# Kernel optimization log

Measured on AMD Instinct MI355X. Metric: run time of the kernel, lower is better.

The kernel has to match this reference:

```python
import jax, jax.numpy as jnp
import numpy as np

E = 8      # num_experts
D = 1024   # input_size
H = 1024   # head_size
K = 2      # top-k


def setup_inputs() -> dict:
    key = jax.random.key(0)
    k1, k2, k3, k4, k5, k6 = jax.random.split(key, 6)
    x = jax.random.normal(k1, (4, 1024, D), dtype=jnp.float32)
    # ParallelExperts init: uniform(-1/fan_in, 1/fan_in)
    w1 = jax.random.uniform(k2, (E, D, H), jnp.float32, -1.0 / D, 1.0 / D)
    b1 = jax.random.uniform(k3, (E, H), jnp.float32, -1.0 / np.sqrt(D), 1.0 / np.sqrt(D))
    w2 = jax.random.uniform(k4, (E, H, D), jnp.float32, -1.0 / H, 1.0 / H)
    b2 = jax.random.uniform(k5, (E, D), jnp.float32, -1.0 / np.sqrt(H), 1.0 / np.sqrt(H))
    # gate Linear(input_size, num_experts, bias=False); scaled so softmax isn't saturated
    wg = jax.random.normal(k6, (D, E), dtype=jnp.float32) * 0.02
    return {"x": x, "w1": w1, "b1": b1, "w2": w2, "b2": b2, "wg": wg}


def reference(x, w1, b1, w2, b2, wg):
    bsz, length, d = x.shape
    xf = x.reshape(-1, d)                                  # [T, D]
    # --- top_k_gating (noisy_gating=False, no skip_mask) ---
    logits = xf @ wg                                       # [T, E]
    probs = jax.nn.softmax(logits, axis=-1)
    top_v, top_i = jax.lax.top_k(probs, K)                 # [T, K]
    top_v = top_v / (jnp.sum(top_v, axis=-1, keepdims=True) + 1e-6)
    # dense combine weights: gate[t, e] = renormalized prob if e in top-k else 0
    gates = jnp.sum(jax.nn.one_hot(top_i, E, dtype=xf.dtype) * top_v[..., None], axis=1)  # [T, E]
    # --- map: per-expert first GEMM + bias (dense formulation == grouped GEMM, no drops) ---
    h = jnp.einsum('td,edh->teh', xf, w1) + b1[None]       # [T, E, H]
    # --- activation between map and reduce (nn.GELU, exact erf form) ---
    a = jax.nn.gelu(h, approximate=False)
    # --- reduce: per-expert second GEMM + bias, scaled by gate, scatter-add back ---
    o = jnp.einsum('teh,ehd->ted', a, w2) + b2[None]       # [T, E, D]
    y = jnp.einsum('te,ted->td', gates, o)                 # [T, D]
    return y.reshape(bsz, length, d)
```

## Files before the change

### kernel.cpp

```cpp
#include <hip/hip_runtime.h>
#include <hip/hip_bf16.h>
#include <math.h>

#define TT 4096
#define EE 8
#define DD 1024
#define HH 1024
#define CAP 4096

typedef __attribute__((ext_vector_type(8))) short bf16x8;
typedef __attribute__((ext_vector_type(4))) float f32x4;

#define GLL16(gp, lp)                                                                   \
    __builtin_amdgcn_global_load_lds((__attribute__((address_space(1))) void*)(gp),     \
                                     (__attribute__((address_space(3))) void*)(lp),     \
                                     16, 0, 0)

static const size_t OFF_XB     = 0;
static const size_t OFF_W1T    = 8u * 1024 * 1024;
static const size_t OFF_W2T    = 24u * 1024 * 1024;
static const size_t OFF_ABUF   = 40u * 1024 * 1024;
static const size_t OFF_OBUF   = 56u * 1024 * 1024;
static const size_t OFF_ROWMAP = 88u * 1024 * 1024;
static const size_t OFF_GATES  = OFF_ROWMAP + 8 * CAP * 4;
static const size_t OFF_COUNTS = OFF_GATES + 8192 * 4;
static const size_t OFF_PICKS  = OFF_COUNTS + 256;

#define NGATE 1024

__global__ __launch_bounds__(256) void prep_kernel(
    const float* __restrict__ x, const float* __restrict__ wg,
    const float* __restrict__ w1, const float* __restrict__ w2,
    __hip_bfloat16* __restrict__ xb,
    __hip_bfloat16* __restrict__ w1t, __hip_bfloat16* __restrict__ w2t,
    int* __restrict__ picks, float* __restrict__ gates)
{
    __shared__ float tl[64][65];
    const int bid = blockIdx.x;
    const int tid = threadIdx.x;

    if (bid >= NGATE) {
        const int bt = bid - NGATE;
        const int mat = bt >> 8;
        const int tt = bt & 255;
        const int R = (tt >> 4) * 64;
        const int C = (tt & 15) * 64;
        const float* src = (mat < EE ? w1 : w2) + (size_t)(mat & 7) * DD * HH;
        __hip_bfloat16* dst = (mat < EE ? w1t : w2t) + (size_t)(mat & 7) * DD * HH;

        const int lrow = tid >> 4;
        const int c4 = tid & 15;
#pragma unroll
        for (int i = 0; i < 4; ++i) {
            const int r = lrow + i * 16;
            float4 v = *(const float4*)(src + (size_t)(R + r) * 1024 + C + c4 * 4);
            tl[r][c4 * 4 + 0] = v.x;
            tl[r][c4 * 4 + 1] = v.y;
            tl[r][c4 * 4 + 2] = v.z;
            tl[r][c4 * 4 + 3] = v.w;
        }
        __syncthreads();
        const int seg = tid & 7;
        const int orow0 = tid >> 3;
#pragma unroll
        for (int p = 0; p < 2; ++p) {
            const int orow = orow0 + p * 32;
            unsigned short u[8];
#pragma unroll
            for (int j = 0; j < 8; ++j) {
                __hip_bfloat16 h = __float2bfloat16(tl[seg * 8 + j][orow]);
                u[j] = *(unsigned short*)&h;
            }
            *(ushort4*)(dst + (size_t)(C + orow) * 1024 + R + seg * 8)     = (ushort4){u[0], u[1], u[2], u[3]};
            *(ushort4*)(dst + (size_t)(C + orow) * 1024 + R + seg * 8 + 4) = (ushort4){u[4], u[5], u[6], u[7]};
        }
        return;
    }

    const int lane = tid & 63;
    const int wave = tid >> 6;
    const int t = bid * 4 + wave;
    {
        const float4* xr = (const float4*)(x + (size_t)t * DD);
        ushort4* xbr = (ushort4*)(xb + (size_t)t * DD);

        float acc[EE];
#pragma unroll
        for (int e = 0; e < EE; ++e) acc[e] = 0.f;

#pragma unroll
        for (int c = 0; c < 4; ++c) {
            const int v4 = lane + 64 * c;
            float4 xv = xr[v4];
            __hip_bfloat16 h0 = __float2bfloat16(xv.x);
            __hip_bfloat16 h1 = __float2bfloat16(xv.y);
            __hip_bfloat16 h2 = __float2bfloat16(xv.z);
            __hip_bfloat16 h3 = __float2bfloat16(xv.w);
            ushort4 s;
            s.x = *(unsigned short*)&h0; s.y = *(unsigned short*)&h1;
            s.z = *(unsigned short*)&h2; s.w = *(unsigned short*)&h3;
            xbr[v4] = s;
            const float4* wrow = (const float4*)(wg + (size_t)(4 * v4) * EE);
            const float xs[4] = {xv.x, xv.y, xv.z, xv.w};
#pragma unroll
            for (int q = 0; q < 4; ++q) {
                float4 w0 = wrow[q * 2];
                float4 w1v = wrow[q * 2 + 1];
                acc[0] = fmaf(xs[q], w0.x, acc[0]);
                acc[1] = fmaf(xs[q], w0.y, acc[1]);
                acc[2] = fmaf(xs[q], w0.z, acc[2]);
                acc[3] = fmaf(xs[q], w0.w, acc[3]);
                acc[4] = fmaf(xs[q], w1v.x, acc[4]);
                acc[5] = fmaf(xs[q], w1v.y, acc[5]);
                acc[6] = fmaf(xs[q], w1v.z, acc[6]);
                acc[7] = fmaf(xs[q], w1v.w, acc[7]);
            }
        }
#pragma unroll
        for (int off = 32; off > 0; off >>= 1) {
#pragma unroll
            for (int e = 0; e < EE; ++e) acc[e] += __shfl_xor(acc[e], off, 64);
        }
        if (lane == 0) {
            float mx = acc[0];
#pragma unroll
            for (int e = 1; e < EE; ++e) mx = fmaxf(mx, acc[e]);
            float p[EE];
            float s = 0.f;
#pragma unroll
            for (int e = 0; e < EE; ++e) { p[e] = expf(acc[e] - mx); s += p[e]; }
            int i0 = 0;
#pragma unroll
            for (int e = 1; e < EE; ++e) if (acc[e] > acc[i0]) i0 = e;
            int i1 = (i0 == 0) ? 1 : 0;
#pragma unroll
            for (int e = 0; e < EE; ++e) {
                if (e != i0 && acc[e] > acc[i1]) i1 = e;
            }
            float v0 = p[i0] / s, v1 = p[i1] / s;
            float den = v0 + v1 + 1e-6f;
            gates[t * 2 + 0] = v0 / den;
            gates[t * 2 + 1] = v1 / den;
            picks[t] = i0 | (i1 << 4);
        }
    }
}

__global__ __launch_bounds__(256) void bucket_build(
    const int* __restrict__ picks, int* __restrict__ rowmap, int* __restrict__ counts)
{
    const int e = blockIdx.x;
    const int tid = threadIdx.x;
    const int lane = tid & 63;
    const int wave = tid >> 6;
    __shared__ int wsum[4];

    int runtot = 0;
    for (int tb = 0; tb < TT; tb += 256) {
        const int t = tb + tid;
        const int p = picks[t];
        const int m0 = ((p & 15) == e) ? 1 : 0;
        const int m1 = (((p >> 4) & 15) == e) ? 1 : 0;
        const int c = m0 + m1;
        int incl = c;
#pragma unroll
        for (int off = 1; off < 64; off <<= 1) {
            int v = __shfl_up(incl, off, 64);
            if (lane >= off) incl += v;
        }
        if (lane == 63) wsum[wave] = incl;
        __syncthreads();
        int wbase = 0;
#pragma unroll
        for (int w = 0; w < 4; ++w) wbase += (w < wave) ? wsum[w] : 0;
        int slot = runtot + wbase + incl - c;
        if (m0) { rowmap[e * CAP + slot] = t * 2; slot += 1; }
        if (m1) { rowmap[e * CAP + slot] = t * 2 + 1; }
        runtot += wsum[0] + wsum[1] + wsum[2] + wsum[3];
        __syncthreads();
    }
    if (tid == 0) counts[e] = runtot;
}

template <int LAYER>
__global__ __launch_bounds__(512) void moe_gemm(
    const __hip_bfloat16* __restrict__ Abase,
    const __hip_bfloat16* __restrict__ Bbase,
    const float* __restrict__ bias,
    const int* __restrict__ rowmap,
    const int* __restrict__ counts,
    const float* __restrict__ gates,
    void* __restrict__ OutP)
{
    const int bid = blockIdx.x;
    const int e = bid & 7;
    const int n0 = ((bid >> 3) & 7) * 128;
    const int m0 = (bid >> 6) * 128;
    const int cnt = counts[e];
    if (m0 >= cnt) return;
    const int tid = threadIdx.x;
    const int lane = tid & 63;
    const int wave = tid >> 6;
    const int wm = (wave >> 2) * 64;
    const int wn = (wave & 3) * 32;
    const int lrow = lane & 15;
    const int quad = lane >> 4;

    __shared__ __hip_bfloat16 As[2][128 * 32];
    __shared__ __hip_bfloat16 Bs[2][128 * 32];

    const int ar = m0 + (tid >> 2);
    const int ea = rowmap[e * CAP + (ar < cnt ? ar : 0)];
    const size_t srcA = (size_t)(LAYER == 1 ? (ea >> 1) : ea);
    const __hip_bfloat16* gA = Abase + srcA * DD + (tid & 3) * 8;
    const __hip_bfloat16* Bexp = Bbase + (size_t)e * DD * HH;
    const __hip_bfloat16* gB = Bexp + (size_t)(n0 + (tid >> 2)) * DD + (tid & 3) * 8;

    f32x4 acc[4][2];
#pragma unroll
    for (int i = 0; i < 4; ++i)
#pragma unroll
        for (int j = 0; j < 2; ++j) acc[i][j] = (f32x4){0.f, 0.f, 0.f, 0.f};

    for (int kt = 0; kt < DD / 64; ++kt) {
#pragma unroll
        for (int s = 0; s < 2; ++s) {
            const int ko = kt * 64 + s * 32;
            GLL16(gA + ko, (char*)&As[s][0] + wave * 1024);
            GLL16(gB + ko, (char*)&Bs[s][0] + wave * 1024);
        }
        __syncthreads();

#pragma unroll
        for (int s = 0; s < 2; ++s) {
            const bf16x8* Av = (const bf16x8*)&As[s][0];
            const bf16x8* Bv = (const bf16x8*)&Bs[s][0];
            bf16x8 af[4], bfr[2];
#pragma unroll
            for (int i = 0; i < 4; ++i)
                af[i] = Av[(wm + i * 16 + lrow) * 4 + quad];
#pragma unroll
            for (int i = 0; i < 2; ++i)
                bfr[i] = Bv[(wn + i * 16 + lrow) * 4 + quad];
#pragma unroll
            for (int mi = 0; mi < 4; ++mi)
#pragma unroll
                for (int ni = 0; ni < 2; ++ni)
                    acc[mi][ni] = __builtin_amdgcn_mfma_f32_16x16x32_bf16(
                        af[mi], bfr[ni], acc[mi][ni], 0, 0, 0);
        }
        __syncthreads();
    }

    if (LAYER == 1) {
        __hip_bfloat16* abuf = (__hip_bfloat16*)OutP;
#pragma unroll
        for (int mi = 0; mi < 4; ++mi) {
#pragma unroll
            for (int r = 0; r < 4; ++r) {
                const int mrow = wm + mi * 16 + quad * 4 + r;
                const int gm = m0 + mrow;
                if (gm < cnt) {
                    const int ent = rowmap[e * CAP + gm];
                    __hip_bfloat16* orow = abuf + (size_t)ent * HH + n0 + wn + lrow;
#pragma unroll
                    for (int ni = 0; ni < 2; ++ni) {
                        float v = acc[mi][ni][r] + bias[e * HH + n0 + wn + ni * 16 + lrow];
                        v = 0.5f * v * (1.f + erff(v * 0.70710678118654752f));
                        orow[ni * 16] = __float2bfloat16(v);
                    }
                }
            }
        }
    } else {
        float* obuf = (float*)OutP;
#pragma unroll
        for (int mi = 0; mi < 4; ++mi) {
#pragma unroll
            for (int r = 0; r < 4; ++r) {
                const int mrow = wm + mi * 16 + quad * 4 + r;
                const int gm = m0 + mrow;
                if (gm < cnt) {
                    const int ent = rowmap[e * CAP + gm];
                    const float g = gates[ent];
                    float* orow = obuf + (size_t)ent * DD + n0 + wn + lrow;
#pragma unroll
                    for (int ni = 0; ni < 2; ++ni) {
                        float v = acc[mi][ni][r] + bias[e * DD + n0 + wn + ni * 16 + lrow];
                        orow[ni * 16] = v * g;
                    }
                }
            }
        }
    }
}

__global__ __launch_bounds__(256) void combine_kernel(
    const float* __restrict__ obuf, float* __restrict__ y)
{
    const size_t i = (size_t)blockIdx.x * 256 + threadIdx.x;
    const size_t t = i >> 8;
    const size_t c = i & 255;
    const float4* o0 = (const float4*)(obuf + t * 2 * DD);
    float4 a = o0[c];
    float4 b = o0[256 + c];
    float4 r;
    r.x = a.x + b.x; r.y = a.y + b.y; r.z = a.z + b.z; r.w = a.w + b.w;
    ((float4*)y)[i] = r;
}

extern "C" void kernel_launch(void* const* d_in, const int* in_sizes, int n_in,
                              void* d_out, int out_size, void* d_ws, size_t ws_size,
                              hipStream_t stream)
{
    const float* x  = (const float*)d_in[0];
    const float* w1 = (const float*)d_in[1];
    const float* b1 = (const float*)d_in[2];
    const float* w2 = (const float*)d_in[3];
    const float* b2 = (const float*)d_in[4];
    const float* wg = (const float*)d_in[5];
    float* y = (float*)d_out;

    char* ws = (char*)d_ws;
    __hip_bfloat16* xb   = (__hip_bfloat16*)(ws + OFF_XB);
    __hip_bfloat16* w1t  = (__hip_bfloat16*)(ws + OFF_W1T);
    __hip_bfloat16* w2t  = (__hip_bfloat16*)(ws + OFF_W2T);
    __hip_bfloat16* abuf = (__hip_bfloat16*)(ws + OFF_ABUF);
    float* obuf  = (float*)(ws + OFF_OBUF);
    int*   rowmap = (int*)(ws + OFF_ROWMAP);
    float* gates  = (float*)(ws + OFF_GATES);
    int*   counts = (int*)(ws + OFF_COUNTS);
    int*   picks  = (int*)(ws + OFF_PICKS);

    prep_kernel<<<NGATE + 4096, 256, 0, stream>>>(x, wg, w1, w2, xb, w1t, w2t, picks, gates);
    bucket_build<<<EE, 256, 0, stream>>>(picks, rowmap, counts);
    moe_gemm<1><<<(CAP / 128) * 8 * EE, 512, 0, stream>>>(
        xb, w1t, b1, rowmap, counts, gates, (void*)abuf);
    moe_gemm<2><<<(CAP / 128) * 8 * EE, 512, 0, stream>>>(
        abuf, w2t, b2, rowmap, counts, gates, (void*)obuf);
    combine_kernel<<<TT * DD / 4 / 256, 256, 0, stream>>>(obuf, y);
}
```

Baseline: 214.3 us.

## Double-buffer LDS tiles in expert GEMM and vectorize transpose stores

The expert GEMM now uses two LDS buffers. It issues the global-to-LDS loads for the next K tile right after the barrier, so they can overlap the MFMA work on the current tile, and it drops one barrier per iteration. The weight-transpose path also writes eight bf16 values with a single 16-byte store instead of two 8-byte stores. LDS use per block doubles, which may lower occupancy. The compiler may also insert conservative waits on the async LDS loads before the ds_reads, which would limit the overlap.

```diff
diff --git a/kernel.cpp b/kernel.cpp
--- a/kernel.cpp
+++ b/kernel.cpp
@@ -10,6 +10,7 @@
 
 typedef __attribute__((ext_vector_type(8))) short bf16x8;
 typedef __attribute__((ext_vector_type(4))) float f32x4;
+typedef __attribute__((ext_vector_type(8))) unsigned short ushort8;
 
 #define GLL16(gp, lp)                                                                   \
     __builtin_amdgcn_global_load_lds((__attribute__((address_space(1))) void*)(gp),     \
@@ -65,14 +66,13 @@
 #pragma unroll
         for (int p = 0; p < 2; ++p) {
             const int orow = orow0 + p * 32;
-            unsigned short u[8];
+            ushort8 u;
 #pragma unroll
             for (int j = 0; j < 8; ++j) {
                 __hip_bfloat16 h = __float2bfloat16(tl[seg * 8 + j][orow]);
                 u[j] = *(unsigned short*)&h;
             }
-            *(ushort4*)(dst + (size_t)(C + orow) * 1024 + R + seg * 8)     = (ushort4){u[0], u[1], u[2], u[3]};
-            *(ushort4*)(dst + (size_t)(C + orow) * 1024 + R + seg * 8 + 4) = (ushort4){u[4], u[5], u[6], u[7]};
+            *(ushort8*)(dst + (size_t)(C + orow) * 1024 + R + seg * 8) = u;
         }
         return;
     }
@@ -206,8 +206,8 @@
     const int lrow = lane & 15;
     const int quad = lane >> 4;
 
-    __shared__ __hip_bfloat16 As[2][128 * 32];
-    __shared__ __hip_bfloat16 Bs[2][128 * 32];
+    __shared__ __hip_bfloat16 As[2][2][128 * 32];
+    __shared__ __hip_bfloat16 Bs[2][2][128 * 32];
 
     const int ar = m0 + (tid >> 2);
     const int ea = rowmap[e * CAP + (ar < cnt ? ar : 0)];
@@ -222,19 +222,25 @@
 #pragma unroll
         for (int j = 0; j < 2; ++j) acc[i][j] = (f32x4){0.f, 0.f, 0.f, 0.f};
 
+#define STAGE(BUF, KT)                                                      \
+    {                                                                       \
+        _Pragma("unroll") for (int s = 0; s < 2; ++s) {                     \
+            const int ko = (KT) * 64 + s * 32;                              \
+            GLL16(gA + ko, (char*)&As[BUF][s][0] + wave * 1024);            \
+            GLL16(gB + ko, (char*)&Bs[BUF][s][0] + wave * 1024);            \
+        }                                                                   \
+    }
+
+    STAGE(0, 0);
     for (int kt = 0; kt < DD / 64; ++kt) {
+        const int cur = kt & 1;
+        __syncthreads();
+        if (kt < DD / 64 - 1) STAGE(cur ^ 1, kt + 1);
+
 #pragma unroll
         for (int s = 0; s < 2; ++s) {
-            const int ko = kt * 64 + s * 32;
-            GLL16(gA + ko, (char*)&As[s][0] + wave * 1024);
-            GLL16(gB + ko, (char*)&Bs[s][0] + wave * 1024);
-        }
-        __syncthreads();
-
-#pragma unroll
-        for (int s = 0; s < 2; ++s) {
-            const bf16x8* Av = (const bf16x8*)&As[s][0];
-            const bf16x8* Bv = (const bf16x8*)&Bs[s][0];
+            const bf16x8* Av = (const bf16x8*)&As[cur][s][0];
+            const bf16x8* Bv = (const bf16x8*)&Bs[cur][s][0];
             bf16x8 af[4], bfr[2];
 #pragma unroll
             for (int i = 0; i < 4; ++i)
@@ -249,8 +255,8 @@
                     acc[mi][ni] = __builtin_amdgcn_mfma_f32_16x16x32_bf16(
                         af[mi], bfr[ni], acc[mi][ni], 0, 0, 0);
         }
-        __syncthreads();
-    }
+    }
+#undef STAGE
 
     if (LAYER == 1) {
         __hip_bfloat16* abuf = (__hip_bfloat16*)OutP;
```

Measured after the change: 232.0 us. 1.08x slower.

## Overlap W2 transpose with layer-1 GEMM via extra blocks, widen stores

Applied to the files above, without the earlier changes.

The fp32-to-bf16 transpose of the second-layer weights moves out of the prep kernel. It now runs in extra blocks appended to the layer-1 MoE GEMM grid, so it can fill idle CUs, since many GEMM blocks exit early when an expert has fewer rows. Transpose stores are widened to 16-byte writes, and the combine kernel processes two float4 per thread with half the blocks. GEMM shared memory becomes a raw buffer sized for two transpose tiles, which may affect occupancy slightly.

```diff
diff --git a/kernel.cpp b/kernel.cpp
--- a/kernel.cpp
+++ b/kernel.cpp
@@ -10,6 +10,7 @@
 
 typedef __attribute__((ext_vector_type(8))) short bf16x8;
 typedef __attribute__((ext_vector_type(4))) float f32x4;
+typedef __attribute__((ext_vector_type(8))) unsigned short ushort8;
 
 #define GLL16(gp, lp)                                                                   \
     __builtin_amdgcn_global_load_lds((__attribute__((address_space(1))) void*)(gp),     \
@@ -28,11 +29,41 @@
 
 #define NGATE 1024
 
+__device__ __forceinline__ void transpose_tile(
+    const float* __restrict__ src, __hip_bfloat16* __restrict__ dst,
+    int R, int C, float (*tl)[65], int t256)
+{
+    const int lrow = t256 >> 4;
+    const int c4 = t256 & 15;
+#pragma unroll
+    for (int i = 0; i < 4; ++i) {
+        const int r = lrow + i * 16;
+        float4 v = *(const float4*)(src + (size_t)(R + r) * 1024 + C + c4 * 4);
+        tl[r][c4 * 4 + 0] = v.x;
+        tl[r][c4 * 4 + 1] = v.y;
+        tl[r][c4 * 4 + 2] = v.z;
+        tl[r][c4 * 4 + 3] = v.w;
+    }
+    __syncthreads();
+    const int seg = t256 & 7;
+    const int orow0 = t256 >> 3;
+#pragma unroll
+    for (int p = 0; p < 2; ++p) {
+        const int orow = orow0 + p * 32;
+        ushort8 u;
+#pragma unroll
+        for (int j = 0; j < 8; ++j) {
+            __hip_bfloat16 h = __float2bfloat16(tl[seg * 8 + j][orow]);
+            u[j] = *(unsigned short*)&h;
+        }
+        *(ushort8*)(dst + (size_t)(C + orow) * 1024 + R + seg * 8) = u;
+    }
+}
+
 __global__ __launch_bounds__(256) void prep_kernel(
     const float* __restrict__ x, const float* __restrict__ wg,
-    const float* __restrict__ w1, const float* __restrict__ w2,
-    __hip_bfloat16* __restrict__ xb,
-    __hip_bfloat16* __restrict__ w1t, __hip_bfloat16* __restrict__ w2t,
+    const float* __restrict__ w1,
+    __hip_bfloat16* __restrict__ xb, __hip_bfloat16* __restrict__ w1t,
     int* __restrict__ picks, float* __restrict__ gates)
 {
     __shared__ float tl[64][65];
@@ -43,37 +74,8 @@
         const int bt = bid - NGATE;
         const int mat = bt >> 8;
         const int tt = bt & 255;
-        const int R = (tt >> 4) * 64;
-        const int C = (tt & 15) * 64;
-        const float* src = (mat < EE ? w1 : w2) + (size_t)(mat & 7) * DD * HH;
-        __hip_bfloat16* dst = (mat < EE ? w1t : w2t) + (size_t)(mat & 7) * DD * HH;
-
-        const int lrow = tid >> 4;
-        const int c4 = tid & 15;
-#pragma unroll
-        for (int i = 0; i < 4; ++i) {
-            const int r = lrow + i * 16;
-            float4 v = *(const float4*)(src + (size_t)(R + r) * 1024 + C + c4 * 4);
-            tl[r][c4 * 4 + 0] = v.x;
-            tl[r][c4 * 4 + 1] = v.y;
-            tl[r][c4 * 4 + 2] = v.z;
-            tl[r][c4 * 4 + 3] = v.w;
-        }
-        __syncthreads();
-        const int seg = tid & 7;
-        const int orow0 = tid >> 3;
-#pragma unroll
-        for (int p = 0; p < 2; ++p) {
-            const int orow = orow0 + p * 32;
-            unsigned short u[8];
-#pragma unroll
-            for (int j = 0; j < 8; ++j) {
-                __hip_bfloat16 h = __float2bfloat16(tl[seg * 8 + j][orow]);
-                u[j] = *(unsigned short*)&h;
-            }
-            *(ushort4*)(dst + (size_t)(C + orow) * 1024 + R + seg * 8)     = (ushort4){u[0], u[1], u[2], u[3]};
-            *(ushort4*)(dst + (size_t)(C + orow) * 1024 + R + seg * 8 + 4) = (ushort4){u[4], u[5], u[6], u[7]};
-        }
+        transpose_tile(w1 + (size_t)mat * DD * HH, w1t + (size_t)mat * DD * HH,
+                       (tt >> 4) * 64, (tt & 15) * 64, tl, tid);
         return;
     }
 
@@ -190,15 +192,30 @@
     const int* __restrict__ rowmap,
     const int* __restrict__ counts,
     const float* __restrict__ gates,
-    void* __restrict__ OutP)
-{
+    void* __restrict__ OutP,
+    const float* __restrict__ wsrc,
+    __hip_bfloat16* __restrict__ wdst)
+{
+    alignas(16) __shared__ char raw[33280];
     const int bid = blockIdx.x;
+    const int tid = threadIdx.x;
+
+    if (LAYER == 1 && bid >= 2048) {
+        const int half = tid >> 8;
+        const int tile = (bid - 2048) * 2 + half;
+        const int mat = tile >> 8;
+        const int tt = tile & 255;
+        float (*tl)[65] = (float(*)[65])(raw + half * 16640);
+        transpose_tile(wsrc + (size_t)mat * DD * HH, wdst + (size_t)mat * DD * HH,
+                       (tt >> 4) * 64, (tt & 15) * 64, tl, tid & 255);
+        return;
+    }
+
     const int e = bid & 7;
     const int n0 = ((bid >> 3) & 7) * 128;
     const int m0 = (bid >> 6) * 128;
     const int cnt = counts[e];
     if (m0 >= cnt) return;
-    const int tid = threadIdx.x;
     const int lane = tid & 63;
     const int wave = tid >> 6;
     const int wm = (wave >> 2) * 64;
@@ -206,8 +223,8 @@
     const int lrow = lane & 15;
     const int quad = lane >> 4;
 
-    __shared__ __hip_bfloat16 As[2][128 * 32];
-    __shared__ __hip_bfloat16 Bs[2][128 * 32];
+    __hip_bfloat16* As = (__hip_bfloat16*)raw;
+    __hip_bfloat16* Bs = (__hip_bfloat16*)(raw + 16384);
 
     const int ar = m0 + (tid >> 2);
     const int ea = rowmap[e * CAP + (ar < cnt ? ar : 0)];
@@ -226,15 +243,15 @@
 #pragma unroll
         for (int s = 0; s < 2; ++s) {
             const int ko = kt * 64 + s * 32;
-            GLL16(gA + ko, (char*)&As[s][0] + wave * 1024);
-            GLL16(gB + ko, (char*)&Bs[s][0] + wave * 1024);
+            GLL16(gA + ko, As + s * 4096 + wave * 512);
+            GLL16(gB + ko, Bs + s * 4096 + wave * 512);
         }
         __syncthreads();
 
 #pragma unroll
         for (int s = 0; s < 2; ++s) {
-            const bf16x8* Av = (const bf16x8*)&As[s][0];
-            const bf16x8* Bv = (const bf16x8*)&Bs[s][0];
+            const bf16x8* Av = (const bf16x8*)(As + s * 4096);
+            const bf16x8* Bv = (const bf16x8*)(Bs + s * 4096);
             bf16x8 af[4], bfr[2];
 #pragma unroll
             for (int i = 0; i < 4; ++i)
@@ -298,15 +315,18 @@
 __global__ __launch_bounds__(256) void combine_kernel(
     const float* __restrict__ obuf, float* __restrict__ y)
 {
-    const size_t i = (size_t)blockIdx.x * 256 + threadIdx.x;
-    const size_t t = i >> 8;
-    const size_t c = i & 255;
-    const float4* o0 = (const float4*)(obuf + t * 2 * DD);
-    float4 a = o0[c];
-    float4 b = o0[256 + c];
-    float4 r;
-    r.x = a.x + b.x; r.y = a.y + b.y; r.z = a.z + b.z; r.w = a.w + b.w;
-    ((float4*)y)[i] = r;
+#pragma unroll
+    for (int k = 0; k < 2; ++k) {
+        const size_t i = (size_t)blockIdx.x * 512 + k * 256 + threadIdx.x;
+        const size_t t = i >> 8;
+        const size_t c = i & 255;
+        const float4* o0 = (const float4*)(obuf + t * 2 * DD);
+        float4 a = o0[c];
+        float4 b = o0[256 + c];
+        float4 r;
+        r.x = a.x + b.x; r.y = a.y + b.y; r.z = a.z + b.z; r.w = a.w + b.w;
+        ((float4*)y)[i] = r;
+    }
 }
 
 extern "C" void kernel_launch(void* const* d_in, const int* in_sizes, int n_in,
@@ -332,11 +352,11 @@
     int*   counts = (int*)(ws + OFF_COUNTS);
     int*   picks  = (int*)(ws + OFF_PICKS);
 
-    prep_kernel<<<NGATE + 4096, 256, 0, stream>>>(x, wg, w1, w2, xb, w1t, w2t, picks, gates);
+    prep_kernel<<<NGATE + 2048, 256, 0, stream>>>(x, wg, w1, xb, w1t, picks, gates);
     bucket_build<<<EE, 256, 0, stream>>>(picks, rowmap, counts);
-    moe_gemm<1><<<(CAP / 128) * 8 * EE, 512, 0, stream>>>(
-        xb, w1t, b1, rowmap, counts, gates, (void*)abuf);
-    moe_gemm<2><<<(CAP / 128) * 8 * EE, 512, 0, stream>>>(
-        abuf, w2t, b2, rowmap, counts, gates, (void*)obuf);
-    combine_kernel<<<TT * DD / 4 / 256, 256, 0, stream>>>(obuf, y);
-}
+    moe_gemm<1><<<2048 + 1024, 512, 0, stream>>>(
+        xb, w1t, b1, rowmap, counts, gates, (void*)abuf, w2, w2t);
+    moe_gemm<2><<<2048, 512, 0, stream>>>(
+        abuf, w2t, b2, rowmap, counts, gates, (void*)obuf, nullptr, nullptr);
+    combine_kernel<<<TT * DD / 4 / 512, 256, 0, stream>>>(obuf, y);
+}
```

Result: faster. 208.3 us (-2.8%).
